# Optimization experiments

Measured on AMD Instinct MI355X. Metric: run time of the kernel, lower is better.

Reference implementation:

```python
import jax, jax.numpy as jnp
import numpy as np

MASK_FILL = -99999.0  # value used by masked_fill_ in the torch source


def setup_inputs() -> dict:
    key = jax.random.key(0)
    k1, k2, k3, k4, k5, k6, k7 = jax.random.split(key, 7)
    B, S, H = 8, 2048, 1024
    query = jax.random.normal(k1, (B, S, H), dtype=jnp.float32)
    key_t = jax.random.normal(k2, (B, S, H), dtype=jnp.float32)
    value = jax.random.normal(k3, (B, S, H), dtype=jnp.float32)
    mask = jax.random.randint(k4, (B, S), 0, 2, dtype=jnp.int32)
    s = 1.0 / np.sqrt(H)
    Wq = jax.random.uniform(k5, (H, H), dtype=jnp.float32, minval=-s, maxval=s)
    Wk = jax.random.uniform(k6, (H, H), dtype=jnp.float32, minval=-s, maxval=s)
    Wv = jax.random.uniform(k7, (H, H), dtype=jnp.float32, minval=-s, maxval=s)
    return {"query": query, "key": key_t, "value": value,
            "Wq": Wq, "Wk": Wk, "Wv": Wv, "mask": mask}


def reference(query, key, value, Wq, Wk, Wv, mask):
    # Linear(h,h,bias=False): y = x @ W.T
    q = jnp.einsum('bsh,oh->bso', query, Wq)
    k = jnp.einsum('bsh,oh->bso', key, Wk)
    v = jnp.einsum('bsh,oh->bso', value, Wv)
    # score[b,i,j] = q[b,i,:] . k[b,j,:]  (NO 1/sqrt(d) scaling in source)
    score = jnp.einsum('bqh,bkh->bqk', q, k)
    # mask: [B, S_k] -> [B, 1, S_k]; positions where mask==0 get MASK_FILL
    m = mask[:, None, :]
    score = jnp.where(m == 0, jnp.float32(MASK_FILL), score)
    attn = jax.nn.softmax(score, axis=-1)
    context = jnp.einsum('bqk,bkh->bqh', attn, v)
    return context
```

## Files before the change

### kernel.cpp

```cpp
#include <hip/hip_runtime.h>
#include <hip/hip_fp16.h>
#include <math.h>

typedef _Float16 f16;
typedef _Float16 f16x4 __attribute__((ext_vector_type(4)));
typedef _Float16 f16x8 __attribute__((ext_vector_type(8)));
typedef float f32x4 __attribute__((ext_vector_type(4)));

#define GLOAD_LDS16(g, l)                                                                  \
    __builtin_amdgcn_global_load_lds((const __attribute__((address_space(1))) void*)(g),   \
                                     (__attribute__((address_space(3))) void*)(l), 16, 0, 0)

__global__ __launch_bounds__(256) void cast3_kernel(const float* __restrict__ s0,
                                                    const float* __restrict__ s1,
                                                    const float* __restrict__ s2,
                                                    f16* d0, f16* d1, f16* d2, int n4each)
{
    const int z = blockIdx.z;
    const float* src = (z == 0) ? s0 : (z == 1) ? s1 : s2;
    f16* d = (z == 0) ? d0 : (z == 1) ? d1 : d2;
    const int stride = gridDim.x * blockDim.x;
    for (int i = blockIdx.x * blockDim.x + threadIdx.x; i < n4each; i += stride) {
        float4 v = *(const float4*)(src + (long long)i * 4);
        *(f16x4*)(d + (long long)i * 4) = (f16x4){(f16)v.x, (f16)v.y, (f16)v.z, (f16)v.w};
    }
}

template <int OUTF16>
__global__ __launch_bounds__(512, 2) void gemm_nt_k(
    const f16* __restrict__ Ab, const f16* __restrict__ Bb, void* __restrict__ Cb,
    int K, int lda, int ldb, int ldc,
    long long sA, long long sB, long long sC, int gx)
{
    __shared__ __align__(16) f16 As[256 * 64];
    __shared__ __align__(16) f16 Bs[128 * 64];

    const int nwg = gridDim.x;
    const int swz = (blockIdx.x & 7) * (nwg >> 3) + (blockIdx.x >> 3);
    const int bx = swz % gx, by = swz / gx;

    const int z = blockIdx.z;
    const char* pA = (const char*)(Ab + z * sA + (long long)by * 256 * lda);
    const char* pB = (const char*)(Bb + z * sB + (long long)bx * 128 * ldb);
    const long long lda2 = (long long)lda * 2, ldb2 = (long long)ldb * 2;

    const int tid = threadIdx.x;
    const int w = tid >> 6, l = tid & 63;
    const int wr = w >> 1, wc = w & 1;

    f32x4 acc[4][4];
#pragma unroll
    for (int i = 0; i < 4; i++)
#pragma unroll
        for (int j = 0; j < 4; j++) acc[i][j] = (f32x4){0.f, 0.f, 0.f, 0.f};

    const int lr = l & 15;
    const int lkb = (l >> 4) * 16;

#define FRAG_A(row, kbyte)                                                                \
    (*(const f16x8*)((const char*)&As[0] + ((row) * 128) + ((kbyte) ^ (((row) & 7) << 4))))
#define FRAG_B(row, kbyte)                                                                \
    (*(const f16x8*)((const char*)&Bs[0] + ((row) * 128) + ((kbyte) ^ (((row) & 7) << 4))))

    const int nt = K >> 6;
    for (int t = 0; t < nt; ++t) {
        const long long kb = (long long)t * 128;
#pragma unroll
        for (int i = 0; i < 4; i++) {
            const int c = i * 512 + tid;
            const int row = c >> 3;
            const int col = ((c & 7) * 16) ^ ((row & 7) << 4);
            GLOAD_LDS16(pA + (long long)row * lda2 + kb + col, &As[(long long)c * 8]);
        }
#pragma unroll
        for (int i = 0; i < 2; i++) {
            const int c = i * 512 + tid;
            const int row = c >> 3;
            const int col = ((c & 7) * 16) ^ ((row & 7) << 4);
            GLOAD_LDS16(pB + (long long)row * ldb2 + kb + col, &Bs[(long long)c * 8]);
        }
        __syncthreads();

        f16x8 bf[4][2], af[4][2];
#pragma unroll
        for (int fc = 0; fc < 4; fc++)
#pragma unroll
            for (int ks = 0; ks < 2; ks++)
                bf[fc][ks] = FRAG_B(wc * 64 + fc * 16 + lr, ks * 64 + lkb);
#pragma unroll
        for (int fq = 0; fq < 4; fq++)
#pragma unroll
            for (int ks = 0; ks < 2; ks++)
                af[fq][ks] = FRAG_A(wr * 64 + fq * 16 + lr, ks * 64 + lkb);

#pragma unroll
        for (int fq = 0; fq < 4; fq++)
#pragma unroll
            for (int fc = 0; fc < 4; fc++)
#pragma unroll
                for (int ks = 0; ks < 2; ks++)
                    acc[fq][fc] = __builtin_amdgcn_mfma_f32_16x16x32_f16(
                        af[fq][ks], bf[fc][ks], acc[fq][fc], 0, 0, 0);

        __syncthreads();
    }
#undef FRAG_A
#undef FRAG_B

    const int row_l = (l >> 4) * 4;
    const long long gr0 = (long long)by * 256 + wr * 64;
    const int gc0 = bx * 128 + wc * 64;
    if (OUTF16) {
        f16* C = (f16*)Cb + z * sC;
#pragma unroll
        for (int fq = 0; fq < 4; fq++)
#pragma unroll
            for (int fc = 0; fc < 4; fc++)
#pragma unroll
                for (int i = 0; i < 4; i++)
                    C[(gr0 + fq * 16 + row_l + i) * ldc + gc0 + fc * 16 + lr] = (f16)acc[fq][fc][i];
    } else {
        float* C = (float*)Cb + z * sC;
#pragma unroll
        for (int fq = 0; fq < 4; fq++)
#pragma unroll
            for (int fc = 0; fc < 4; fc++)
#pragma unroll
                for (int i = 0; i < 4; i++)
                    C[(gr0 + fq * 16 + row_l + i) * ldc + gc0 + fc * 16 + lr] = acc[fq][fc][i];
    }
}

__global__ __launch_bounds__(256) void transpose_v_kernel(const f16* __restrict__ v, f16* __restrict__ vT)
{
    __shared__ f16 tile[64][72];
    const int b = blockIdx.z;
    const int s0 = blockIdx.x * 64, o0 = blockIdx.y * 64;
    const int t = threadIdx.x;
    const int r = t >> 2, c = (t & 3) * 16;
    const f16* src = v + ((long long)b * 2048 + s0) * 1024 + o0;
    *(f16x8*)&tile[r][c]     = *(const f16x8*)(src + (long long)r * 1024 + c);
    *(f16x8*)&tile[r][c + 8] = *(const f16x8*)(src + (long long)r * 1024 + c + 8);
    __syncthreads();
    f16* dst = vT + ((long long)b * 1024 + o0) * 2048 + s0;
    f16 buf[16];
#pragma unroll
    for (int j = 0; j < 16; j++) buf[j] = tile[c + j][r];
    *(f16x8*)(dst + (long long)r * 2048 + c)     = *(f16x8*)&buf[0];
    *(f16x8*)(dst + (long long)r * 2048 + c + 8) = *(f16x8*)&buf[8];
}

__device__ __forceinline__ float wred_max(float v) {
#pragma unroll
    for (int o = 32; o > 0; o >>= 1) v = fmaxf(v, __shfl_xor(v, o));
    return v;
}
__device__ __forceinline__ float wred_sum(float v) {
#pragma unroll
    for (int o = 32; o > 0; o >>= 1) v += __shfl_xor(v, o);
    return v;
}

__global__ __launch_bounds__(256) void softmax_kernel(f16* __restrict__ Sm, const int* __restrict__ mask)
{
    const long long row = blockIdx.x;
    const int b = (int)(row >> 11);
    f16* Srow = Sm + row * 2048;
    const int* mrow = mask + b * 2048;
    const int t = threadIdx.x;
    const int w = t >> 6, l = t & 63;

    f16x8 sv = *(const f16x8*)(Srow + t * 8);
    int4 m0 = *(const int4*)(mrow + t * 8);
    int4 m1 = *(const int4*)(mrow + t * 8 + 4);
    int mk[8] = {m0.x, m0.y, m0.z, m0.w, m1.x, m1.y, m1.z, m1.w};
    float v[8];
#pragma unroll
    for (int j = 0; j < 8; j++) v[j] = (float)sv[j];

    float mx = -INFINITY;
#pragma unroll
    for (int j = 0; j < 8; j++) if (mk[j]) mx = fmaxf(mx, v[j]);
    mx = wred_max(mx);
    __shared__ float redm[4], reds[4];
    if (l == 0) redm[w] = mx;
    __syncthreads();
    mx = fmaxf(fmaxf(redm[0], redm[1]), fmaxf(redm[2], redm[3]));

    if (mx == -INFINITY) {
        const f16 u = (f16)(1.0f / 2048.0f);
        f16x8 pv;
#pragma unroll
        for (int j = 0; j < 8; j++) pv[j] = u;
        *(f16x8*)(Srow + t * 8) = pv;
        return;
    }

    float e[8];
    float s = 0.f;
#pragma unroll
    for (int j = 0; j < 8; j++) { e[j] = mk[j] ? expf(v[j] - mx) : 0.f; s += e[j]; }
    s = wred_sum(s);
    if (l == 0) reds[w] = s;
    __syncthreads();
    s = reds[0] + reds[1] + reds[2] + reds[3];
    const float inv = 1.0f / s;
    f16x8 pv;
#pragma unroll
    for (int j = 0; j < 8; j++) pv[j] = (f16)(e[j] * inv);
    *(f16x8*)(Srow + t * 8) = pv;
}

extern "C" void kernel_launch(void* const* d_in, const int* in_sizes, int n_in,
                              void* d_out, int out_size, void* d_ws, size_t ws_size,
                              hipStream_t stream)
{
    const float* query = (const float*)d_in[0];
    const float* keyi  = (const float*)d_in[1];
    const float* value = (const float*)d_in[2];
    const float* Wq    = (const float*)d_in[3];
    const float* Wk    = (const float*)d_in[4];
    const float* Wv    = (const float*)d_in[5];
    const int*   mask  = (const int*)d_in[6];
    float* out = (float*)d_out;

    const long long SH = (long long)8 * 2048 * 1024;
    f16* slot0 = (f16*)d_ws;
    f16* slot1 = slot0 + SH;
    f16* slot2 = slot0 + 2 * SH;
    f16* slot3 = slot0 + 3 * SH;
    f16* slot4 = slot0 + 4 * SH;
    f16* wh    = slot4;
    f16* Pb    = slot0;

    const int n4x = (int)(SH / 4);
    const int n4w = 1024 * 1024 / 4;
    const long long zero = 0;
    const long long M1 = 1024 * 1024;

    cast3_kernel<<<dim3(128, 1, 3), 256, 0, stream>>>(Wq, Wk, Wv, wh, wh + M1, wh + 2 * M1, n4w);
    cast3_kernel<<<dim3(2048, 1, 3), 256, 0, stream>>>(query, keyi, value, slot3, slot0, slot1, n4x);
    gemm_nt_k<1><<<dim3(512, 1, 1), 512, 0, stream>>>(
        slot3, wh, (void*)slot2, 1024, 1024, 1024, 1024, zero, zero, zero, 8);
    gemm_nt_k<1><<<dim3(512, 1, 1), 512, 0, stream>>>(
        slot0, wh + M1, (void*)slot3, 1024, 1024, 1024, 1024, zero, zero, zero, 8);
    gemm_nt_k<1><<<dim3(512, 1, 1), 512, 0, stream>>>(
        slot1, wh + 2 * M1, (void*)slot0, 1024, 1024, 1024, 1024, zero, zero, zero, 8);
    transpose_v_kernel<<<dim3(32, 16, 8), 256, 0, stream>>>(slot0, slot4);
    gemm_nt_k<1><<<dim3(128, 1, 8), 512, 0, stream>>>(
        slot2, slot3, (void*)Pb, 1024, 1024, 1024, 2048,
        (long long)2048 * 1024, (long long)2048 * 1024, (long long)2048 * 2048, 16);
    softmax_kernel<<<dim3(16384), 256, 0, stream>>>(Pb, mask);
    gemm_nt_k<0><<<dim3(64, 1, 8), 512, 0, stream>>>(
        Pb, slot4, (void*)out, 2048, 2048, 2048, 1024,
        (long long)2048 * 2048, (long long)1024 * 2048, (long long)2048 * 1024, 8);
}
```

Baseline: 332.6 us.

## Fuse V transpose into the V projection GEMM epilogue via LDS staging

The V projection GEMM now writes its output already transposed (vT layout). It stages each 128-row half of the accumulator tile through shared memory and stores contiguous 16-byte chunks, so the separate transpose kernel and its full read and write of V are gone. The fp32-to-fp16 cast kernel also processes 16 elements per thread with 16-byte stores. Workspace slots are reassigned to fit. The epilogue adds extra barriers and LDS traffic to the V GEMM.

Measured after the change: 325.2 us. 1.02x faster.

```diff
diff --git a/kernel.cpp b/kernel.cpp
--- a/kernel.cpp
+++ b/kernel.cpp
@@ -14,26 +14,32 @@
 __global__ __launch_bounds__(256) void cast3_kernel(const float* __restrict__ s0,
                                                     const float* __restrict__ s1,
                                                     const float* __restrict__ s2,
-                                                    f16* d0, f16* d1, f16* d2, int n4each)
+                                                    f16* d0, f16* d1, f16* d2, int n16each)
 {
     const int z = blockIdx.z;
     const float* src = (z == 0) ? s0 : (z == 1) ? s1 : s2;
-    f16* d = (z == 0) ? d0 : (z == 1) ? d1 : d2;
+    f16* dst = (z == 0) ? d0 : (z == 1) ? d1 : d2;
     const int stride = gridDim.x * blockDim.x;
-    for (int i = blockIdx.x * blockDim.x + threadIdx.x; i < n4each; i += stride) {
-        float4 v = *(const float4*)(src + (long long)i * 4);
-        *(f16x4*)(d + (long long)i * 4) = (f16x4){(f16)v.x, (f16)v.y, (f16)v.z, (f16)v.w};
-    }
-}
-
-template <int OUTF16>
+    for (int i = blockIdx.x * blockDim.x + threadIdx.x; i < n16each; i += stride) {
+        const float4* sp = (const float4*)(src + (long long)i * 16);
+        float4 a = sp[0], b = sp[1], c = sp[2], d4 = sp[3];
+        f16x8 lo = {(f16)a.x, (f16)a.y, (f16)a.z, (f16)a.w,
+                    (f16)b.x, (f16)b.y, (f16)b.z, (f16)b.w};
+        f16x8 hi = {(f16)c.x, (f16)c.y, (f16)c.z, (f16)c.w,
+                    (f16)d4.x, (f16)d4.y, (f16)d4.z, (f16)d4.w};
+        f16x8* dp = (f16x8*)(dst + (long long)i * 16);
+        dp[0] = lo;
+        dp[1] = hi;
+    }
+}
+
+template <int OUTF16, int TRANSC>
 __global__ __launch_bounds__(512, 2) void gemm_nt_k(
     const f16* __restrict__ Ab, const f16* __restrict__ Bb, void* __restrict__ Cb,
     int K, int lda, int ldb, int ldc,
     long long sA, long long sB, long long sC, int gx)
 {
-    __shared__ __align__(16) f16 As[256 * 64];
-    __shared__ __align__(16) f16 Bs[128 * 64];
+    __shared__ __align__(16) f16 smem[256 * 64 + 128 * 64];
 
     const int nwg = gridDim.x;
     const int swz = (blockIdx.x & 7) * (nwg >> 3) + (blockIdx.x >> 3);
@@ -58,9 +64,9 @@
     const int lkb = (l >> 4) * 16;
 
 #define FRAG_A(row, kbyte)                                                                \
-    (*(const f16x8*)((const char*)&As[0] + ((row) * 128) + ((kbyte) ^ (((row) & 7) << 4))))
+    (*(const f16x8*)((const char*)&smem[0] + ((row) * 128) + ((kbyte) ^ (((row) & 7) << 4))))
 #define FRAG_B(row, kbyte)                                                                \
-    (*(const f16x8*)((const char*)&Bs[0] + ((row) * 128) + ((kbyte) ^ (((row) & 7) << 4))))
+    (*(const f16x8*)((const char*)&smem[0] + 32768 + ((row) * 128) + ((kbyte) ^ (((row) & 7) << 4))))
 
     const int nt = K >> 6;
     for (int t = 0; t < nt; ++t) {
@@ -70,14 +76,14 @@
             const int c = i * 512 + tid;
             const int row = c >> 3;
             const int col = ((c & 7) * 16) ^ ((row & 7) << 4);
-            GLOAD_LDS16(pA + (long long)row * lda2 + kb + col, &As[(long long)c * 8]);
+            GLOAD_LDS16(pA + (long long)row * lda2 + kb + col, &smem[(long long)c * 8]);
         }
 #pragma unroll
         for (int i = 0; i < 2; i++) {
             const int c = i * 512 + tid;
             const int row = c >> 3;
             const int col = ((c & 7) * 16) ^ ((row & 7) << 4);
-            GLOAD_LDS16(pB + (long long)row * ldb2 + kb + col, &Bs[(long long)c * 8]);
+            GLOAD_LDS16(pB + (long long)row * ldb2 + kb + col, &smem[16384 + (long long)c * 8]);
         }
         __syncthreads();
 
@@ -110,7 +116,36 @@
     const int row_l = (l >> 4) * 4;
     const long long gr0 = (long long)by * 256 + wr * 64;
     const int gc0 = bx * 128 + wc * 64;
-    if (OUTF16) {
+
+    if (TRANSC) {
+        const long long blk_r0 = (long long)by * 256;
+        const int b = (int)(blk_r0 >> 11);
+        const int s_base = (int)(blk_r0 & 2047);
+        f16* vTp = (f16*)Cb + (long long)b * 1024 * 2048;
+#pragma unroll
+        for (int h = 0; h < 2; h++) {
+            __syncthreads();
+            if ((wr >> 1) == h) {
+                const int s64 = (wr & 1) * 64;
+#pragma unroll
+                for (int fq = 0; fq < 4; fq++)
+#pragma unroll
+                    for (int fc = 0; fc < 4; fc++)
+#pragma unroll
+                        for (int i = 0; i < 4; i++)
+                            smem[(wc * 64 + fc * 16 + lr) * 136 + s64 + fq * 16 + row_l + i] =
+                                (f16)acc[fq][fc][i];
+            }
+            __syncthreads();
+#pragma unroll
+            for (int j = 0; j < 4; j++) {
+                const int c = j * 512 + tid;
+                const int o = c >> 4, s8 = (c & 15) * 8;
+                f16x8 vv = *(const f16x8*)&smem[o * 136 + s8];
+                *(f16x8*)&vTp[((long long)(bx * 128 + o)) * 2048 + s_base + h * 128 + s8] = vv;
+            }
+        }
+    } else if (OUTF16) {
         f16* C = (f16*)Cb + z * sC;
 #pragma unroll
         for (int fq = 0; fq < 4; fq++)
@@ -129,25 +164,6 @@
                 for (int i = 0; i < 4; i++)
                     C[(gr0 + fq * 16 + row_l + i) * ldc + gc0 + fc * 16 + lr] = acc[fq][fc][i];
     }
-}
-
-__global__ __launch_bounds__(256) void transpose_v_kernel(const f16* __restrict__ v, f16* __restrict__ vT)
-{
-    __shared__ f16 tile[64][72];
-    const int b = blockIdx.z;
-    const int s0 = blockIdx.x * 64, o0 = blockIdx.y * 64;
-    const int t = threadIdx.x;
-    const int r = t >> 2, c = (t & 3) * 16;
-    const f16* src = v + ((long long)b * 2048 + s0) * 1024 + o0;
-    *(f16x8*)&tile[r][c]     = *(const f16x8*)(src + (long long)r * 1024 + c);
-    *(f16x8*)&tile[r][c + 8] = *(const f16x8*)(src + (long long)r * 1024 + c + 8);
-    __syncthreads();
-    f16* dst = vT + ((long long)b * 1024 + o0) * 2048 + s0;
-    f16 buf[16];
-#pragma unroll
-    for (int j = 0; j < 16; j++) buf[j] = tile[c + j][r];
-    *(f16x8*)(dst + (long long)r * 2048 + c)     = *(f16x8*)&buf[0];
-    *(f16x8*)(dst + (long long)r * 2048 + c + 8) = *(f16x8*)&buf[8];
 }
 
 __device__ __forceinline__ float wred_max(float v) {
@@ -230,28 +246,27 @@
     f16* slot2 = slot0 + 2 * SH;
     f16* slot3 = slot0 + 3 * SH;
     f16* slot4 = slot0 + 4 * SH;
-    f16* wh    = slot4;
+    f16* wh    = slot1;
     f16* Pb    = slot0;
 
-    const int n4x = (int)(SH / 4);
-    const int n4w = 1024 * 1024 / 4;
+    const int n16x = (int)(SH / 16);
+    const int n16w = 1024 * 1024 / 16;
     const long long zero = 0;
     const long long M1 = 1024 * 1024;
 
-    cast3_kernel<<<dim3(128, 1, 3), 256, 0, stream>>>(Wq, Wk, Wv, wh, wh + M1, wh + 2 * M1, n4w);
-    cast3_kernel<<<dim3(2048, 1, 3), 256, 0, stream>>>(query, keyi, value, slot3, slot0, slot1, n4x);
-    gemm_nt_k<1><<<dim3(512, 1, 1), 512, 0, stream>>>(
+    cast3_kernel<<<dim3(64, 1, 3), 256, 0, stream>>>(Wq, Wk, Wv, wh, wh + M1, wh + 2 * M1, n16w);
+    cast3_kernel<<<dim3(1024, 1, 3), 256, 0, stream>>>(query, keyi, value, slot3, slot0, slot2, n16x);
+    gemm_nt_k<1, 1><<<dim3(512, 1, 1), 512, 0, stream>>>(
+        slot2, wh + 2 * M1, (void*)slot4, 1024, 1024, 1024, 2048, zero, zero, zero, 8);
+    gemm_nt_k<1, 0><<<dim3(512, 1, 1), 512, 0, stream>>>(
         slot3, wh, (void*)slot2, 1024, 1024, 1024, 1024, zero, zero, zero, 8);
-    gemm_nt_k<1><<<dim3(512, 1, 1), 512, 0, stream>>>(
+    gemm_nt_k<1, 0><<<dim3(512, 1, 1), 512, 0, stream>>>(
         slot0, wh + M1, (void*)slot3, 1024, 1024, 1024, 1024, zero, zero, zero, 8);
-    gemm_nt_k<1><<<dim3(512, 1, 1), 512, 0, stream>>>(
-        slot1, wh + 2 * M1, (void*)slot0, 1024, 1024, 1024, 1024, zero, zero, zero, 8);
-    transpose_v_kernel<<<dim3(32, 16, 8), 256, 0, stream>>>(slot0, slot4);
-    gemm_nt_k<1><<<dim3(128, 1, 8), 512, 0, stream>>>(
+    gemm_nt_k<1, 0><<<dim3(128, 1, 8), 512, 0, stream>>>(
         slot2, slot3, (void*)Pb, 1024, 1024, 1024, 2048,
         (long long)2048 * 1024, (long long)2048 * 1024, (long long)2048 * 2048, 16);
     softmax_kernel<<<dim3(16384), 256, 0, stream>>>(Pb, mask);
-    gemm_nt_k<0><<<dim3(64, 1, 8), 512, 0, stream>>>(
+    gemm_nt_k<0, 0><<<dim3(64, 1, 8), 512, 0, stream>>>(
         Pb, slot4, (void*)out, 2048, 2048, 2048, 1024,
         (long long)2048 * 2048, (long long)1024 * 2048, (long long)2048 * 1024, 8);
 }
```
